# Kernel tuning notes

Measured on AMD Instinct MI355X. Metric: run time of the kernel, lower is better.

Reference implementation:

```python
import jax, jax.numpy as jnp
import numpy as np

B, L, D, H = 4, 2048, 1024, 16
HD = D // H

def setup_inputs() -> dict:
    key = jax.random.key(0)
    ks = jax.random.split(key, 5)
    s = 1.0 / np.sqrt(D)
    return {
        "x": jax.random.normal(ks[0], (B, L, D), dtype=jnp.float32),
        "W_qkv": jax.random.normal(ks[1], (D, 3 * D), dtype=jnp.float32) * s,
        "b_qkv": jnp.zeros((3 * D,), dtype=jnp.float32),
        "W_proj": jax.random.normal(ks[2], (D, D), dtype=jnp.float32) * s,
        "b_proj": jnp.zeros((D,), dtype=jnp.float32),
    }

def reference(x, W_qkv, b_qkv, W_proj, b_proj):
    Bx, Lx, Dx = x.shape
    qkv = x @ W_qkv + b_qkv                      # [B,L,3D]
    q, k, v = jnp.split(qkv, 3, axis=-1)
    # [B,L,D] -> [B,H,L,hd]
    def heads(t):
        return t.reshape(Bx, Lx, H, HD).transpose(0, 2, 1, 3)
    q, k, v = heads(q), heads(k), heads(v)
    scale = 1.0 / np.sqrt(HD)
    scores = jnp.einsum('bhqd,bhkd->bhqk', q, k) * scale   # [B,H,L,L]
    causal = jnp.tril(jnp.ones((Lx, Lx), dtype=bool))
    scores = jnp.where(causal[None, None], scores, -jnp.inf)
    probs = jax.nn.softmax(scores, axis=-1)
    y = jnp.einsum('bhqk,bhkd->bhqd', probs, v)             # [B,H,L,hd]
    y = y.transpose(0, 2, 1, 3).reshape(Bx, Lx, Dx)
    return y @ W_proj + b_proj
```

## Files before the change

### kernel.cpp

```cpp
#include <hip/hip_runtime.h>
#include <stdint.h>

#define DEV __device__ __forceinline__

typedef uint32_t u32;
typedef uint16_t u16;
typedef __attribute__((ext_vector_type(4))) float f32x4;
typedef __attribute__((ext_vector_type(8))) __bf16 bf16x8;

DEV u16 f32_to_bf16(float f) {
  u32 u = __builtin_bit_cast(u32, f);
  u += 0x7FFFu + ((u >> 16) & 1u);
  return (u16)(u >> 16);
}
DEV float bf16_to_f32(u16 h) {
  u32 u = ((u32)h) << 16;
  return __builtin_bit_cast(float, u);
}
DEV bf16x8 load_frag16(const u16* p) {
  return __builtin_bit_cast(bf16x8, *(const uint4*)p);
}
DEV float exp2_fast(float x) {
#if __has_builtin(__builtin_amdgcn_exp2f)
  return __builtin_amdgcn_exp2f(x);
#else
  float r;
  asm("v_exp_f32 %0, %1\n\ts_nop 0" : "=v"(r) : "v"(x));
  return r;
#endif
}
DEV u32 cvt_pk_bf16(float lo, float hi) {
  u32 r;
  asm("v_cvt_pk_bf16_f32 %0, %1, %2" : "=v"(r) : "v"(lo), "v"(hi));
  return r;
}

DEV void gl_lds16(const u16* g, u16* l) {
  __builtin_amdgcn_global_load_lds(
      (__attribute__((address_space(1))) void*)(u16*)g,
      (__attribute__((address_space(3))) void*)l, 16, 0, 0);
}

DEV const u16* swz(const u16* basep, int row, int colByte) {
  return (const u16*)((const char*)basep + row * 128 + (colByte ^ ((row & 7) << 4)));
}
DEV u16* swzw(u16* basep, int row, int colByte) {
  return (u16*)((char*)basep + row * 128 + (colByte ^ ((row & 7) << 4)));
}

__global__ void cvt_f32_bf16(const float* __restrict__ in, u16* __restrict__ out, int n) {
  int i = (blockIdx.x * 256 + threadIdx.x) * 4;
  if (i >= n) return;
  float4 v = *(const float4*)(in + i);
  ushort4 o;
  o.x = f32_to_bf16(v.x); o.y = f32_to_bf16(v.y);
  o.z = f32_to_bf16(v.z); o.w = f32_to_bf16(v.w);
  *(ushort4*)(out + i) = o;
}

__global__ void transpose_cvt(const float* __restrict__ in, u16* __restrict__ out, int R, int C) {
  __shared__ float tile[32][33];
  int bx = blockIdx.x * 32;
  int by = blockIdx.y * 32;
  int tx = threadIdx.x & 31;
  int ty = threadIdx.x >> 5;
#pragma unroll
  for (int i = 0; i < 32; i += 8)
    tile[ty + i][tx] = in[(size_t)(by + ty + i) * C + bx + tx];
  __syncthreads();
#pragma unroll
  for (int i = 0; i < 32; i += 8)
    out[(size_t)(bx + ty + i) * R + by + tx] = f32_to_bf16(tile[tx][ty + i]);
}

__global__ void transpose_v(const u16* __restrict__ qkvb, u16* __restrict__ vTg) {
  const int LDT = 72;
  __shared__ __attribute__((aligned(16))) u16 t[64 * 72];
  int bh = blockIdx.y;
  int b = bh >> 4, h = bh & 15;
  int l0 = blockIdx.x * 64;
  int tid = threadIdx.x;
#pragma unroll
  for (int p = 0; p < 2; ++p) {
    int chunk = p * 256 + tid;
    int row = chunk >> 3, cc = chunk & 7;
    *(uint4*)(t + row * LDT + cc * 8) =
        *(const uint4*)(qkvb + (size_t)(b * 2048 + l0 + row) * 3072 + 2048 + h * 64 + cc * 8);
  }
  __syncthreads();
#pragma unroll
  for (int p = 0; p < 2; ++p) {
    int chunk = p * 256 + tid;
    int d = chunk >> 3, cc = chunk & 7;
    ushort4 o0, o1;
    o0.x = t[(cc * 8 + 0) * LDT + d]; o0.y = t[(cc * 8 + 1) * LDT + d];
    o0.z = t[(cc * 8 + 2) * LDT + d]; o0.w = t[(cc * 8 + 3) * LDT + d];
    o1.x = t[(cc * 8 + 4) * LDT + d]; o1.y = t[(cc * 8 + 5) * LDT + d];
    o1.z = t[(cc * 8 + 6) * LDT + d]; o1.w = t[(cc * 8 + 7) * LDT + d];
    u16* op = vTg + ((size_t)bh * 64 + d) * 2048 + l0;
    *(ushort4*)(op + cc * 8 + 0) = o0;
    *(ushort4*)(op + cc * 8 + 4) = o1;
  }
}

template <int OUT_BF16>
__global__ __launch_bounds__(256, 2) void gemm_bf16(
    const u16* __restrict__ A, const u16* __restrict__ Bt,
    const float* __restrict__ bias, void* __restrict__ Cout,
    int M, int N, int K) {
  __shared__ __attribute__((aligned(16))) u16 As[128 * 64];
  __shared__ __attribute__((aligned(16))) u16 Bs[128 * 64];
  int tid = threadIdx.x;
  int m0 = blockIdx.y * 128;
  int n0 = blockIdx.x * 128;
  int w = tid >> 6, l = tid & 63;
  int wr = w >> 1, wc = w & 1;
  int lr = l & 15, lg = l >> 4;
  int rloc = l >> 3, cc = l & 7;
  int scc8 = (cc ^ rloc) * 8;

  f32x4 acc[4][4];
#pragma unroll
  for (int i = 0; i < 4; i++)
#pragma unroll
    for (int j = 0; j < 4; j++) acc[i][j] = (f32x4)0.0f;

  for (int kt = 0; kt < K; kt += 64) {
    __syncthreads();
#pragma unroll
    for (int qq = 0; qq < 4; ++qq) {
      int row = 32 * w + 8 * qq + rloc;
      gl_lds16(A + (size_t)(m0 + row) * K + kt + scc8, &As[(32 * w + 8 * qq) * 64]);
      gl_lds16(Bt + (size_t)(n0 + row) * K + kt + scc8, &Bs[(32 * w + 8 * qq) * 64]);
    }
    __syncthreads();
#pragma unroll
    for (int kk = 0; kk < 2; ++kk) {
      bf16x8 af[4], bfr[4];
#pragma unroll
      for (int i = 0; i < 4; i++)
        af[i] = load_frag16(swz(As, wr * 64 + i * 16 + lr, kk * 64 + lg * 16));
#pragma unroll
      for (int j = 0; j < 4; j++)
        bfr[j] = load_frag16(swz(Bs, wc * 64 + j * 16 + lr, kk * 64 + lg * 16));
#pragma unroll
      for (int i = 0; i < 4; i++)
#pragma unroll
        for (int j = 0; j < 4; j++)
          acc[i][j] = __builtin_amdgcn_mfma_f32_16x16x32_bf16(af[i], bfr[j], acc[i][j], 0, 0, 0);
    }
  }
#pragma unroll
  for (int i = 0; i < 4; i++) {
#pragma unroll
    for (int j = 0; j < 4; j++) {
      int col = n0 + wc * 64 + j * 16 + lr;
      float bv = bias[col];
#pragma unroll
      for (int r = 0; r < 4; r++) {
        int row = m0 + wr * 64 + i * 16 + lg * 4 + r;
        float v = acc[i][j][r] + bv;
        if (OUT_BF16)
          ((u16*)Cout)[(size_t)row * N + col] = f32_to_bf16(v);
        else
          ((float*)Cout)[(size_t)row * N + col] = v;
      }
    }
  }
}

__global__ __launch_bounds__(256, 2) void attn_kernel(
    const u16* __restrict__ qkvb, const u16* __restrict__ vTg,
    u16* __restrict__ attnb) {
  __shared__ __attribute__((aligned(16))) u16 Ks[2][64 * 64];
  __shared__ __attribute__((aligned(16))) u16 Vt[2][64 * 64];
  __shared__ __attribute__((aligned(16))) u16 Pl[4][32 * 64];
  int tid = threadIdx.x;
  int w = tid >> 6, l = tid & 63;
  int lr = l & 15, lg = l >> 4;
  int rloc = l >> 3, cc = l & 7;
  int scc8 = (cc ^ rloc) * 8;
  int bh = blockIdx.y;
  int b = bh >> 4, h = bh & 15;
  const u16* base = qkvb + (size_t)b * 2048 * 3072;
  const u16* kglob = base + 1024 + h * 64;
  const u16* vbase = vTg + (size_t)bh * 64 * 2048;
  u16* PlW = Pl[w];
  const float SCALE = 0.18033688011112042f;

#define STAGE_KV(bi, tt)                                                        \
  do {                                                                          \
    int kv0_ = (tt) * 64;                                                       \
    _Pragma("unroll")                                                           \
    for (int qq = 0; qq < 2; ++qq) {                                            \
      int row_ = 16 * w + 8 * qq + rloc;                                        \
      gl_lds16(kglob + (size_t)(kv0_ + row_) * 3072 + scc8,                     \
               &Ks[bi][(16 * w + 8 * qq) * 64]);                                \
      gl_lds16(vbase + (size_t)row_ * 2048 + kv0_ + scc8,                       \
               &Vt[bi][(16 * w + 8 * qq) * 64]);                                \
    }                                                                           \
  } while (0)

  for (int half = 0; half < 2; ++half) {
    int s = half ? 15 - (int)blockIdx.x : (int)blockIdx.x;
    int qb = s * 128;
    int nkv = 2 * s + 2;
    int tmax = 2 * s + (w >> 1);

    bf16x8 qf[2][2];
#pragma unroll
    for (int i = 0; i < 2; i++)
#pragma unroll
      for (int kk = 0; kk < 2; kk++) {
        int row = qb + w * 32 + i * 16 + lr;
        uint4 v = *(const uint4*)(base + (size_t)row * 3072 + h * 64 + kk * 32 + lg * 8);
        u32 wd[4] = {v.x, v.y, v.z, v.w};
#pragma unroll
        for (int e = 0; e < 4; e++) {
          float flo = bf16_to_f32((u16)(wd[e] & 0xFFFFu)) * SCALE;
          float fhi = bf16_to_f32((u16)(wd[e] >> 16)) * SCALE;
          wd[e] = cvt_pk_bf16(flo, fhi);
        }
        uint4 sv; sv.x = wd[0]; sv.y = wd[1]; sv.z = wd[2]; sv.w = wd[3];
        qf[i][kk] = __builtin_bit_cast(bf16x8, sv);
      }

    float m_st[2] = {-1e30f, -1e30f};
    float l_st[2] = {0.f, 0.f};
    f32x4 of[2][4];
#pragma unroll
    for (int i = 0; i < 2; i++)
#pragma unroll
      for (int j = 0; j < 4; j++) of[i][j] = (f32x4)0.0f;

    STAGE_KV(0, 0);

    for (int t = 0; t < nkv; ++t) {
      int cur = t & 1;
      __syncthreads();
      if (t + 1 < nkv) STAGE_KV(cur ^ 1, t + 1);

      if (t <= tmax) {
        const u16* Kb = Ks[cur];
        const u16* Vb = Vt[cur];

        f32x4 St[4][2];
#pragma unroll
        for (int j = 0; j < 4; j++)
#pragma unroll
          for (int i = 0; i < 2; i++) St[j][i] = (f32x4)0.0f;
        __builtin_amdgcn_s_setprio(1);
#pragma unroll
        for (int kk = 0; kk < 2; ++kk) {
          bf16x8 kbf[4];
#pragma unroll
          for (int j = 0; j < 4; j++)
            kbf[j] = load_frag16(swz(Kb, j * 16 + lr, kk * 64 + lg * 16));
#pragma unroll
          for (int j = 0; j < 4; j++)
#pragma unroll
            for (int i = 0; i < 2; i++)
              St[j][i] = __builtin_amdgcn_mfma_f32_16x16x32_bf16(kbf[j], qf[i][kk], St[j][i], 0, 0, 0);
        }
        __builtin_amdgcn_s_setprio(0);

        if (t == tmax) {
#pragma unroll
          for (int j = 0; j < 4; j++)
#pragma unroll
            for (int i = 0; i < 2; i++)
#pragma unroll
              for (int r = 0; r < 4; r++) {
                int kabs = t * 64 + j * 16 + lg * 4 + r;
                int qabs = qb + w * 32 + i * 16 + lr;
                if (kabs > qabs) St[j][i][r] = -1e30f;
              }
        }

#pragma unroll
        for (int i = 0; i < 2; ++i) {
          float tm = -1e30f;
#pragma unroll
          for (int j = 0; j < 4; j++)
#pragma unroll
            for (int r = 0; r < 4; r++) tm = fmaxf(tm, St[j][i][r]);
          tm = fmaxf(tm, __shfl_xor(tm, 16));
          tm = fmaxf(tm, __shfl_xor(tm, 32));
          if (!__all((int)(tm <= m_st[i] + 10.0f))) {
            float mn = fmaxf(m_st[i], tm);
            float fsc = exp2_fast(m_st[i] - mn);
            m_st[i] = mn;
            l_st[i] *= fsc;
#pragma unroll
            for (int r = 0; r < 4; ++r) {
              float ff = __shfl(fsc, lg * 4 + r);
#pragma unroll
              for (int jd = 0; jd < 4; jd++) of[i][jd][r] *= ff;
            }
          }
          float rs = 0.f;
#pragma unroll
          for (int j = 0; j < 4; ++j) {
            float p0 = exp2_fast(St[j][i][0] - m_st[i]);
            float p1 = exp2_fast(St[j][i][1] - m_st[i]);
            float p2 = exp2_fast(St[j][i][2] - m_st[i]);
            float p3 = exp2_fast(St[j][i][3] - m_st[i]);
            rs += (p0 + p1) + (p2 + p3);
            uint2 pk;
            pk.x = cvt_pk_bf16(p0, p1);
            pk.y = cvt_pk_bf16(p2, p3);
            *(uint2*)swzw(PlW, i * 16 + lr, j * 32 + lg * 8) = pk;
          }
          rs += __shfl_xor(rs, 16);
          rs += __shfl_xor(rs, 32);
          l_st[i] += rs;
        }

        __builtin_amdgcn_s_setprio(1);
#pragma unroll
        for (int ks = 0; ks < 2; ++ks) {
          bf16x8 ap[2], vbf[4];
#pragma unroll
          for (int i = 0; i < 2; i++)
            ap[i] = load_frag16(swz(PlW, i * 16 + lr, ks * 64 + lg * 16));
#pragma unroll
          for (int jd = 0; jd < 4; jd++)
            vbf[jd] = load_frag16(swz(Vb, jd * 16 + lr, ks * 64 + lg * 16));
#pragma unroll
          for (int i = 0; i < 2; i++)
#pragma unroll
            for (int jd = 0; jd < 4; jd++)
              of[i][jd] = __builtin_amdgcn_mfma_f32_16x16x32_bf16(ap[i], vbf[jd], of[i][jd], 0, 0, 0);
        }
        __builtin_amdgcn_s_setprio(0);
      }
    }
    __syncthreads();

#pragma unroll
    for (int i = 0; i < 2; i++) {
#pragma unroll
      for (int r = 0; r < 4; r++) {
        float ls = __shfl(l_st[i], lg * 4 + r);
        float inv = 1.0f / ls;
#pragma unroll
        for (int jd = 0; jd < 4; jd++) {
          int row = qb + w * 32 + i * 16 + lg * 4 + r;
          int col = h * 64 + jd * 16 + lr;
          attnb[((size_t)b * 2048 + row) * 1024 + col] = f32_to_bf16(of[i][jd][r] * inv);
        }
      }
    }
  }
#undef STAGE_KV
}

extern "C" void kernel_launch(void* const* d_in, const int* in_sizes, int n_in,
                              void* d_out, int out_size, void* d_ws, size_t ws_size,
                              hipStream_t stream) {
  const float* x = (const float*)d_in[0];
  const float* Wqkv = (const float*)d_in[1];
  const float* bqkv = (const float*)d_in[2];
  const float* Wproj = (const float*)d_in[3];
  const float* bproj = (const float*)d_in[4];
  float* out = (float*)d_out;

  char* ws = (char*)d_ws;
  u16* xb    = (u16*)(ws);
  u16* vTg   = (u16*)(ws);
  u16* wqT   = (u16*)(ws + 16777216);
  u16* wpT   = (u16*)(ws + 23068672);
  u16* qkvb  = (u16*)(ws + 25165824);
  u16* attnb = (u16*)(ws + 75497472);

  cvt_f32_bf16<<<8192, 256, 0, stream>>>(x, xb, 8388608);
  transpose_cvt<<<dim3(96, 32), 256, 0, stream>>>(Wqkv, wqT, 1024, 3072);
  transpose_cvt<<<dim3(32, 32), 256, 0, stream>>>(Wproj, wpT, 1024, 1024);
  gemm_bf16<1><<<dim3(24, 64), 256, 0, stream>>>(xb, wqT, bqkv, (void*)qkvb, 8192, 3072, 1024);
  transpose_v<<<dim3(32, 64), 256, 0, stream>>>(qkvb, vTg);
  attn_kernel<<<dim3(8, 64), 256, 0, stream>>>(qkvb, vTg, attnb);
  gemm_bf16<0><<<dim3(8, 64), 256, 0, stream>>>(attnb, wpT, bproj, (void*)out, 8192, 1024, 1024);
}
```

Baseline: 174.4 us.

## Stage 128-row KV tiles in attention and remap workgroups for XCD locality

The attention kernel now stages K and V in 128-row chunks, double-buffered, and processes two 64-row sub-tiles per stage. This halves the number of block-wide barriers and staging rounds per query block. Both the GEMM and attention kernels remap the linear workgroup id so that neighbouring tiles land on the same XCD, aiming for better L2 reuse. The larger LDS footprint (about 80KB per block) may lower occupancy below the 2 blocks per CU that launch_bounds requests.

Result: faster. 165.1 us (-5.3%).

```diff
diff --git a/kernel.cpp b/kernel.cpp
--- a/kernel.cpp
+++ b/kernel.cpp
@@ -111,8 +111,11 @@
   __shared__ __attribute__((aligned(16))) u16 As[128 * 64];
   __shared__ __attribute__((aligned(16))) u16 Bs[128 * 64];
   int tid = threadIdx.x;
-  int m0 = blockIdx.y * 128;
-  int n0 = blockIdx.x * 128;
+  u32 nwg = gridDim.x * gridDim.y;
+  u32 orig = blockIdx.y * gridDim.x + blockIdx.x;
+  u32 wg = (orig & 7) * (nwg >> 3) + (orig >> 3);
+  int m0 = (wg / gridDim.x) * 128;
+  int n0 = (wg % gridDim.x) * 128;
   int w = tid >> 6, l = tid & 63;
   int wr = w >> 1, wc = w & 1;
   int lr = l & 15, lg = l >> 4;
@@ -172,40 +175,44 @@
 __global__ __launch_bounds__(256, 2) void attn_kernel(
     const u16* __restrict__ qkvb, const u16* __restrict__ vTg,
     u16* __restrict__ attnb) {
-  __shared__ __attribute__((aligned(16))) u16 Ks[2][64 * 64];
-  __shared__ __attribute__((aligned(16))) u16 Vt[2][64 * 64];
+  __shared__ __attribute__((aligned(16))) u16 Ks[2][2 * 64 * 64];
+  __shared__ __attribute__((aligned(16))) u16 Vt[2][2 * 64 * 64];
   __shared__ __attribute__((aligned(16))) u16 Pl[4][32 * 64];
   int tid = threadIdx.x;
   int w = tid >> 6, l = tid & 63;
   int lr = l & 15, lg = l >> 4;
   int rloc = l >> 3, cc = l & 7;
   int scc8 = (cc ^ rloc) * 8;
-  int bh = blockIdx.y;
+  u32 orig = blockIdx.y * 8 + blockIdx.x;
+  u32 wg = (orig & 7) * 64 + (orig >> 3);
+  int bx = wg & 7;
+  int bh = wg >> 3;
   int b = bh >> 4, h = bh & 15;
   const u16* base = qkvb + (size_t)b * 2048 * 3072;
   const u16* kglob = base + 1024 + h * 64;
   const u16* vbase = vTg + (size_t)bh * 64 * 2048;
   u16* PlW = Pl[w];
+  int usub = w >> 1, wl = w & 1;
   const float SCALE = 0.18033688011112042f;
 
-#define STAGE_KV(bi, tt)                                                        \
+#define STAGE128(bi, tt)                                                        \
   do {                                                                          \
-    int kv0_ = (tt) * 64;                                                       \
+    int kv0_ = (tt) * 128;                                                      \
     _Pragma("unroll")                                                           \
-    for (int qq = 0; qq < 2; ++qq) {                                            \
-      int row_ = 16 * w + 8 * qq + rloc;                                        \
-      gl_lds16(kglob + (size_t)(kv0_ + row_) * 3072 + scc8,                     \
-               &Ks[bi][(16 * w + 8 * qq) * 64]);                                \
-      gl_lds16(vbase + (size_t)row_ * 2048 + kv0_ + scc8,                       \
-               &Vt[bi][(16 * w + 8 * qq) * 64]);                                \
+    for (int qq = 0; qq < 4; ++qq) {                                            \
+      int lrow_ = 32 * wl + 8 * qq;            \
+      gl_lds16(kglob + (size_t)(kv0_ + usub * 64 + lrow_ + rloc) * 3072 + scc8, \
+               &Ks[bi][usub * 4096 + lrow_ * 64]);                              \
+      gl_lds16(vbase + (size_t)(lrow_ + rloc) * 2048 + kv0_ + usub * 64 + scc8, \
+               &Vt[bi][usub * 4096 + lrow_ * 64]);                              \
     }                                                                           \
   } while (0)
 
   for (int half = 0; half < 2; ++half) {
-    int s = half ? 15 - (int)blockIdx.x : (int)blockIdx.x;
+    int s = half ? 15 - bx : bx;
     int qb = s * 128;
-    int nkv = 2 * s + 2;
-    int tmax = 2 * s + (w >> 1);
+    int nst = s + 1;
+    int tmax64 = 2 * s + (w >> 1);
 
     bf16x8 qf[2][2];
 #pragma unroll
@@ -233,106 +240,110 @@
 #pragma unroll
       for (int j = 0; j < 4; j++) of[i][j] = (f32x4)0.0f;
 
-    STAGE_KV(0, 0);
-
-    for (int t = 0; t < nkv; ++t) {
+    STAGE128(0, 0);
+
+    for (int t = 0; t < nst; ++t) {
       int cur = t & 1;
       __syncthreads();
-      if (t + 1 < nkv) STAGE_KV(cur ^ 1, t + 1);
-
-      if (t <= tmax) {
-        const u16* Kb = Ks[cur];
-        const u16* Vb = Vt[cur];
-
-        f32x4 St[4][2];
-#pragma unroll
-        for (int j = 0; j < 4; j++)
-#pragma unroll
-          for (int i = 0; i < 2; i++) St[j][i] = (f32x4)0.0f;
-        __builtin_amdgcn_s_setprio(1);
-#pragma unroll
-        for (int kk = 0; kk < 2; ++kk) {
-          bf16x8 kbf[4];
+      if (t + 1 < nst) STAGE128(cur ^ 1, t + 1);
+
+#pragma unroll
+      for (int u = 0; u < 2; ++u) {
+        int t64 = 2 * t + u;
+        if (t64 <= tmax64) {
+          const u16* Kb = Ks[cur] + u * 4096;
+          const u16* Vb = Vt[cur] + u * 4096;
+
+          f32x4 St[4][2];
 #pragma unroll
           for (int j = 0; j < 4; j++)
-            kbf[j] = load_frag16(swz(Kb, j * 16 + lr, kk * 64 + lg * 16));
-#pragma unroll
-          for (int j = 0; j < 4; j++)
+#pragma unroll
+            for (int i = 0; i < 2; i++) St[j][i] = (f32x4)0.0f;
+          __builtin_amdgcn_s_setprio(1);
+#pragma unroll
+          for (int kk = 0; kk < 2; ++kk) {
+            bf16x8 kbf[4];
+#pragma unroll
+            for (int j = 0; j < 4; j++)
+              kbf[j] = load_frag16(swz(Kb, j * 16 + lr, kk * 64 + lg * 16));
+#pragma unroll
+            for (int j = 0; j < 4; j++)
+#pragma unroll
+              for (int i = 0; i < 2; i++)
+                St[j][i] = __builtin_amdgcn_mfma_f32_16x16x32_bf16(kbf[j], qf[i][kk], St[j][i], 0, 0, 0);
+          }
+          __builtin_amdgcn_s_setprio(0);
+
+          if (t64 == tmax64) {
+#pragma unroll
+            for (int j = 0; j < 4; j++)
+#pragma unroll
+              for (int i = 0; i < 2; i++)
+#pragma unroll
+                for (int r = 0; r < 4; r++) {
+                  int kabs = t64 * 64 + j * 16 + lg * 4 + r;
+                  int qabs = qb + w * 32 + i * 16 + lr;
+                  if (kabs > qabs) St[j][i][r] = -1e30f;
+                }
+          }
+
+#pragma unroll
+          for (int i = 0; i < 2; ++i) {
+            float tm = -1e30f;
+#pragma unroll
+            for (int j = 0; j < 4; j++)
+#pragma unroll
+              for (int r = 0; r < 4; r++) tm = fmaxf(tm, St[j][i][r]);
+            tm = fmaxf(tm, __shfl_xor(tm, 16));
+            tm = fmaxf(tm, __shfl_xor(tm, 32));
+            if (!__all((int)(tm <= m_st[i] + 10.0f))) {
+              float mn = fmaxf(m_st[i], tm);
+              float fsc = exp2_fast(m_st[i] - mn);
+              m_st[i] = mn;
+              l_st[i] *= fsc;
+#pragma unroll
+              for (int r = 0; r < 4; ++r) {
+                float ff = __shfl(fsc, lg * 4 + r);
+#pragma unroll
+                for (int jd = 0; jd < 4; jd++) of[i][jd][r] *= ff;
+              }
+            }
+            float rs = 0.f;
+#pragma unroll
+            for (int j = 0; j < 4; ++j) {
+              float p0 = exp2_fast(St[j][i][0] - m_st[i]);
+              float p1 = exp2_fast(St[j][i][1] - m_st[i]);
+              float p2 = exp2_fast(St[j][i][2] - m_st[i]);
+              float p3 = exp2_fast(St[j][i][3] - m_st[i]);
+              rs += (p0 + p1) + (p2 + p3);
+              uint2 pk;
+              pk.x = cvt_pk_bf16(p0, p1);
+              pk.y = cvt_pk_bf16(p2, p3);
+              *(uint2*)swzw(PlW, i * 16 + lr, j * 32 + lg * 8) = pk;
+            }
+            rs += __shfl_xor(rs, 16);
+            rs += __shfl_xor(rs, 32);
+            l_st[i] += rs;
+          }
+
+          __builtin_amdgcn_s_setprio(1);
+#pragma unroll
+          for (int ks = 0; ks < 2; ++ks) {
+            bf16x8 ap[2], vbf[4];
 #pragma unroll
             for (int i = 0; i < 2; i++)
-              St[j][i] = __builtin_amdgcn_mfma_f32_16x16x32_bf16(kbf[j], qf[i][kk], St[j][i], 0, 0, 0);
+              ap[i] = load_frag16(swz(PlW, i * 16 + lr, ks * 64 + lg * 16));
+#pragma unroll
+            for (int jd = 0; jd < 4; jd++)
+              vbf[jd] = load_frag16(swz(Vb, jd * 16 + lr, ks * 64 + lg * 16));
+#pragma unroll
+            for (int i = 0; i < 2; i++)
+#pragma unroll
+              for (int jd = 0; jd < 4; jd++)
+                of[i][jd] = __builtin_amdgcn_mfma_f32_16x16x32_bf16(ap[i], vbf[jd], of[i][jd], 0, 0, 0);
+          }
+          __builtin_amdgcn_s_setprio(0);
         }
-        __builtin_amdgcn_s_setprio(0);
-
-        if (t == tmax) {
-#pragma unroll
-          for (int j = 0; j < 4; j++)
-#pragma unroll
-            for (int i = 0; i < 2; i++)
-#pragma unroll
-              for (int r = 0; r < 4; r++) {
-                int kabs = t * 64 + j * 16 + lg * 4 + r;
-                int qabs = qb + w * 32 + i * 16 + lr;
-                if (kabs > qabs) St[j][i][r] = -1e30f;
-              }
-        }
-
-#pragma unroll
-        for (int i = 0; i < 2; ++i) {
-          float tm = -1e30f;
-#pragma unroll
-          for (int j = 0; j < 4; j++)
-#pragma unroll
-            for (int r = 0; r < 4; r++) tm = fmaxf(tm, St[j][i][r]);
-          tm = fmaxf(tm, __shfl_xor(tm, 16));
-          tm = fmaxf(tm, __shfl_xor(tm, 32));
-          if (!__all((int)(tm <= m_st[i] + 10.0f))) {
-            float mn = fmaxf(m_st[i], tm);
-            float fsc = exp2_fast(m_st[i] - mn);
-            m_st[i] = mn;
-            l_st[i] *= fsc;
-#pragma unroll
-            for (int r = 0; r < 4; ++r) {
-              float ff = __shfl(fsc, lg * 4 + r);
-#pragma unroll
-              for (int jd = 0; jd < 4; jd++) of[i][jd][r] *= ff;
-            }
-          }
-          float rs = 0.f;
-#pragma unroll
-          for (int j = 0; j < 4; ++j) {
-            float p0 = exp2_fast(St[j][i][0] - m_st[i]);
-            float p1 = exp2_fast(St[j][i][1] - m_st[i]);
-            float p2 = exp2_fast(St[j][i][2] - m_st[i]);
-            float p3 = exp2_fast(St[j][i][3] - m_st[i]);
-            rs += (p0 + p1) + (p2 + p3);
-            uint2 pk;
-            pk.x = cvt_pk_bf16(p0, p1);
-            pk.y = cvt_pk_bf16(p2, p3);
-            *(uint2*)swzw(PlW, i * 16 + lr, j * 32 + lg * 8) = pk;
-          }
-          rs += __shfl_xor(rs, 16);
-          rs += __shfl_xor(rs, 32);
-          l_st[i] += rs;
-        }
-
-        __builtin_amdgcn_s_setprio(1);
-#pragma unroll
-        for (int ks = 0; ks < 2; ++ks) {
-          bf16x8 ap[2], vbf[4];
-#pragma unroll
-          for (int i = 0; i < 2; i++)
-            ap[i] = load_frag16(swz(PlW, i * 16 + lr, ks * 64 + lg * 16));
-#pragma unroll
-          for (int jd = 0; jd < 4; jd++)
-            vbf[jd] = load_frag16(swz(Vb, jd * 16 + lr, ks * 64 + lg * 16));
-#pragma unroll
-          for (int i = 0; i < 2; i++)
-#pragma unroll
-            for (int jd = 0; jd < 4; jd++)
-              of[i][jd] = __builtin_amdgcn_mfma_f32_16x16x32_bf16(ap[i], vbf[jd], of[i][jd], 0, 0, 0);
-        }
-        __builtin_amdgcn_s_setprio(0);
       }
     }
     __syncthreads();
@@ -352,7 +363,7 @@
       }
     }
   }
-#undef STAGE_KV
+#undef STAGE128
 }
 
 extern "C" void kernel_launch(void* const* d_in, const int* in_sizes, int n_in,
```
